# Kernel optimization log

Measured on AMD Instinct MI355X. Metric: run time of the kernel, lower is better.

Reference implementation:

```python
import jax, jax.numpy as jnp
import numpy as np

HEAD_DIM = 64
NUM_HEADS = 32
ROPE_BASE = 10000.0


def _rope_interleaved(x):
    # x: [B, T, H, D]; interleaved RoPE on query, seqlen_offset = 0
    B, T, H, D = x.shape
    inv_freq = 1.0 / (ROPE_BASE ** (jnp.arange(0, D, 2, dtype=jnp.float32) / D))  # [D/2]
    t = jnp.arange(T, dtype=jnp.float32)
    freqs = t[:, None] * inv_freq[None, :]          # [T, D/2]
    cos = jnp.cos(freqs)[None, :, None, :]          # [1, T, 1, D/2]
    sin = jnp.sin(freqs)[None, :, None, :]
    x1 = x[..., 0::2]
    x2 = x[..., 1::2]
    o1 = x1 * cos - x2 * sin
    o2 = x1 * sin + x2 * cos
    out = jnp.stack([o1, o2], axis=-1).reshape(x.shape)  # re-interleave
    return out


def setup_inputs() -> dict:
    key = jax.random.key(0)
    k1, k2, k3, k4, k5 = jax.random.split(key, 5)
    B, T, Dm = 2, 2048, 2048
    H, Dh = NUM_HEADS, HEAD_DIM
    scale = 0.02
    return {
        "hidden_states": jax.random.normal(k1, (B, T, Dm), jnp.float32),
        "shared_k": jax.random.normal(k2, (B, T, H, Dh), jnp.float32),
        "shared_v": jax.random.normal(k3, (B, T, H, Dh), jnp.float32),
        "Wq": jax.random.normal(k4, (Dm, Dm), jnp.float32) * scale,
        "Wo": jax.random.normal(k5, (Dm, Dm), jnp.float32) * scale,
    }


def reference(hidden_states, shared_k, shared_v, Wq, Wo):
    B, T, Dm = hidden_states.shape
    H, Dh = NUM_HEADS, HEAD_DIM
    # q projection (nn.Linear: x @ W.T)
    q = (hidden_states @ Wq.T).reshape(B, T, H, Dh)
    # rotary on q only (seqlen_offset = shared_k_len - q_len = 0)
    q = _rope_interleaved(q)
    # parallel causal attention over shared KV cache (window_size=None)
    scale = 1.0 / jnp.sqrt(jnp.asarray(Dh, jnp.float32))
    scores = jnp.einsum('bqhd,bkhd->bhqk', q, shared_k) * scale
    causal = jnp.tril(jnp.ones((T, T), dtype=bool))
    scores = jnp.where(causal[None, None], scores, -jnp.inf)
    p = jax.nn.softmax(scores, axis=-1)
    o = jnp.einsum('bhqk,bkhd->bqhd', p, shared_v)
    o = o.reshape(B, T, Dm)
    return o @ Wo.T
```

## Files before the change

### kernel.cpp

```cpp
#include <hip/hip_runtime.h>
#include <stdint.h>

typedef short short8 __attribute__((ext_vector_type(8)));
typedef float f32x4 __attribute__((ext_vector_type(4)));
typedef int int2v __attribute__((ext_vector_type(2)));
typedef int int4v __attribute__((ext_vector_type(4)));

#define QSCALE 0.1803368801111137f
#define FREQC 0.4152410118609203f

__device__ __forceinline__ float bf2f(unsigned short u) {
    union { unsigned int i; float f; } x; x.i = ((unsigned int)u) << 16; return x.f;
}
__device__ __forceinline__ unsigned short f2bf(float f) {
    union { float f; unsigned int i; } x; x.f = f;
    unsigned int i = x.i;
    unsigned int r = i + 0x7FFFu + ((i >> 16) & 1u);
    return (unsigned short)(r >> 16);
}
__device__ __forceinline__ ushort4 cvt4(float4 v) {
    ushort4 o;
    o.x = f2bf(v.x); o.y = f2bf(v.y); o.z = f2bf(v.z); o.w = f2bf(v.w);
    return o;
}
__device__ __forceinline__ int cvtpk_bf16(float lo, float hi) {
    int r;
    asm("v_cvt_pk_bf16_f32 %0, %1, %2" : "=v"(r) : "v"(lo), "v"(hi));
    return r;
}

#define GLDS16(g, l) \
    __builtin_amdgcn_global_load_lds((const __attribute__((address_space(1))) void*)(g), \
                                     (__attribute__((address_space(3))) void*)(l), 16, 0, 0)

#define WAITVM(n) asm volatile("s_waitcnt vmcnt(" #n ")" ::: "memory")

__global__ __launch_bounds__(256) void cvt_tr(
    const float* __restrict__ hs, const float* __restrict__ k,
    const float* __restrict__ wq, const float* __restrict__ wo,
    const float* __restrict__ V,
    unsigned short* __restrict__ hs_b, unsigned short* __restrict__ k_b,
    unsigned short* __restrict__ wq_b, unsigned short* __restrict__ wo_b,
    unsigned short* __restrict__ Vt) {
    __shared__ float s[64 * 65];
    int blk = blockIdx.x;
    int tid = threadIdx.x;
    if (blk < 2048) {
        size_t base = (size_t)blk * 256 + tid;
        const float4* inh = (const float4*)hs;
        const float4* ink = (const float4*)k;
        const float4* inq = (const float4*)wq;
        const float4* ino = (const float4*)wo;
        ushort4* outh = (ushort4*)hs_b;
        ushort4* outk = (ushort4*)k_b;
        ushort4* outq = (ushort4*)wq_b;
        ushort4* outo = (ushort4*)wo_b;
        {
            float4 v[4];
#pragma unroll
            for (int it = 0; it < 4; ++it) v[it] = inh[(size_t)it * 524288 + base];
#pragma unroll
            for (int it = 0; it < 4; ++it) outh[(size_t)it * 524288 + base] = cvt4(v[it]);
        }
        {
            float4 v[4];
#pragma unroll
            for (int it = 0; it < 4; ++it) v[it] = ink[(size_t)it * 524288 + base];
#pragma unroll
            for (int it = 0; it < 4; ++it) outk[(size_t)it * 524288 + base] = cvt4(v[it]);
        }
        {
            float4 v[2];
#pragma unroll
            for (int it = 0; it < 2; ++it) v[it] = inq[(size_t)it * 524288 + base];
#pragma unroll
            for (int it = 0; it < 2; ++it) outq[(size_t)it * 524288 + base] = cvt4(v[it]);
        }
        {
            float4 v[2];
#pragma unroll
            for (int it = 0; it < 2; ++it) v[it] = ino[(size_t)it * 524288 + base];
#pragma unroll
            for (int it = 0; it < 2; ++it) outo[(size_t)it * 524288 + base] = cvt4(v[it]);
        }
        return;
    }
    int tb = blk - 2048;
    int t0 = (tb & 31) * 64;
    int bh = tb >> 5;
    int b = bh >> 5, h = bh & 31;
#pragma unroll
    for (int it = 0; it < 4; ++it) {
        int c = tid + it * 256;
        int t = c >> 4;
        int d0 = (c & 15) * 4;
        float4 v = *(const float4*)(V + (size_t)(((b * 2048 + t0 + t) * 32 + h)) * 64 + d0);
        s[t * 65 + d0 + 0] = v.x; s[t * 65 + d0 + 1] = v.y;
        s[t * 65 + d0 + 2] = v.z; s[t * 65 + d0 + 3] = v.w;
    }
    __syncthreads();
#pragma unroll
    for (int it = 0; it < 2; ++it) {
        int c = tid + it * 256;
        int d = c >> 3;
        int tt = (c & 7) * 8;
        short8 pk;
#pragma unroll
        for (int j = 0; j < 8; ++j) pk[j] = (short)f2bf(s[(tt + j) * 65 + d]);
        *(short8*)(Vt + (size_t)(bh * 64 + d) * 2048 + t0 + tt) = pk;
    }
}

template <bool BF16_OUT>
__global__ __launch_bounds__(256) void gemm_bt(
    const unsigned short* __restrict__ A,
    const unsigned short* __restrict__ B,
    void* __restrict__ Cout,
    int M, int N, int K)
{
    __shared__ __align__(16) unsigned short lA[2][128 * 64];
    __shared__ __align__(16) unsigned short lB[2][128 * 64];
    int tid = threadIdx.x, lane = tid & 63, wave = tid >> 6;
    int wm = (wave >> 1) * 64, wn = (wave & 1) * 64;
    int m16 = lane & 15, q = lane >> 4;
    int rowBase = blockIdx.x * 128, colBase = blockIdx.y * 128;
    f32x4 acc[4][4] = {};

    int sr = lane >> 3;
    int g  = (lane & 7) ^ sr;
    const unsigned short* gAp = A + (size_t)(rowBase + wave * 32 + sr) * K + g * 8;
    const unsigned short* gBp = B + (size_t)(colBase + wave * 32 + sr) * K + g * 8;

#define GSTAGE(buf, k0)                                                                      \
    do {                                                                                     \
        _Pragma("unroll")                                                                    \
        for (int gi = 0; gi < 4; ++gi) {                                                     \
            GLDS16(gAp + (size_t)(8 * gi) * K + (k0), &lA[buf][(wave * 32 + 8 * gi) * 64]);  \
            GLDS16(gBp + (size_t)(8 * gi) * K + (k0), &lB[buf][(wave * 32 + 8 * gi) * 64]);  \
        }                                                                                    \
    } while (0)

    GSTAGE(0, 0);
    WAITVM(0);
    __builtin_amdgcn_s_barrier();
    int cur = 0;
    for (int k0 = 0; k0 < K; k0 += 64) {
        if (k0 + 64 < K) {
            GSTAGE(cur ^ 1, k0 + 64);
            WAITVM(8);
        } else {
            WAITVM(0);
        }
        __builtin_amdgcn_s_barrier();
        const unsigned short* la = lA[cur];
        const unsigned short* lb = lB[cur];
#pragma unroll
        for (int kk = 0; kk < 2; ++kk) {
            short8 af[4], bfr[4];
#pragma unroll
            for (int i2 = 0; i2 < 4; ++i2) {
                int RA = wm + i2 * 16 + m16;
                af[i2]  = *(const short8*)&la[RA * 64 + (((kk * 4 + q) ^ (RA & 7)) * 8)];
                int RB = wn + i2 * 16 + m16;
                bfr[i2] = *(const short8*)&lb[RB * 64 + (((kk * 4 + q) ^ (RB & 7)) * 8)];
            }
#pragma unroll
            for (int i2 = 0; i2 < 4; ++i2)
#pragma unroll
                for (int jn = 0; jn < 4; ++jn)
                    acc[i2][jn] = __builtin_amdgcn_mfma_f32_16x16x32_bf16(af[i2], bfr[jn], acc[i2][jn], 0, 0, 0);
        }
        __builtin_amdgcn_s_barrier();
        cur ^= 1;
    }
#pragma unroll
    for (int i = 0; i < 4; ++i)
#pragma unroll
        for (int jn = 0; jn < 4; ++jn)
#pragma unroll
            for (int r = 0; r < 4; ++r) {
                int row = rowBase + wm + i * 16 + q * 4 + r;
                int col = colBase + wn + jn * 16 + m16;
                float v = acc[i][jn][r];
                if (BF16_OUT) ((unsigned short*)Cout)[(size_t)row * N + col] = f2bf(v);
                else          ((float*)Cout)[(size_t)row * N + col] = v;
            }
}

__global__ __launch_bounds__(256, 4) void attn(
    const unsigned short* __restrict__ Q,
    const unsigned short* __restrict__ Kb,
    const unsigned short* __restrict__ Vt,
    unsigned short* __restrict__ O)
{
    __shared__ __align__(16) unsigned short sK[2][64 * 64];
    __shared__ __align__(16) unsigned short sV[2][64 * 64];
    int tid = threadIdx.x, lane = tid & 63, w = tid >> 6;
    int m16 = lane & 15, q = lane >> 4;
    int rx = m16 & 7;
    int flat = blockIdx.x;
    int bh = flat & 63, p = flat >> 6;
    int b = bh >> 5, h = bh & 31;
    int qtA = 31 - p, qtB = p;

    short8 aqA0, aqA1, aqB0, aqB1;
    {
        int tA = qtA * 64 + w * 16 + m16;
        int tB = qtB * 64 + w * 16 + m16;
        const unsigned short* rowA = Q + (size_t)(b * 2048 + tA) * 2048 + h * 64 + q * 8;
        const unsigned short* rowB = Q + (size_t)(b * 2048 + tB) * 2048 + h * 64 + q * 8;
        short8 a0 = *(const short8*)rowA, a1 = *(const short8*)(rowA + 32);
        short8 b0 = *(const short8*)rowB, b1 = *(const short8*)(rowB + 32);
        float tfA = (float)tA, tfB = (float)tB;
#pragma unroll
        for (int j = 0; j < 4; ++j) {
            float inv0 = __builtin_amdgcn_exp2f(-FREQC * (float)(q * 4 + j));
            float inv1 = __builtin_amdgcn_exp2f(-FREQC * (float)(16 + q * 4 + j));
            float cA0 = __cosf(tfA * inv0), sA0 = __sinf(tfA * inv0);
            float cA1 = __cosf(tfA * inv1), sA1 = __sinf(tfA * inv1);
            float cB0 = __cosf(tfB * inv0), sB0 = __sinf(tfB * inv0);
            float cB1 = __cosf(tfB * inv1), sB1 = __sinf(tfB * inv1);
            float x1, x2;
            x1 = bf2f((unsigned short)a0[2 * j]); x2 = bf2f((unsigned short)a0[2 * j + 1]);
            aqA0[2 * j]     = (short)f2bf((x1 * cA0 - x2 * sA0) * QSCALE);
            aqA0[2 * j + 1] = (short)f2bf((x1 * sA0 + x2 * cA0) * QSCALE);
            x1 = bf2f((unsigned short)a1[2 * j]); x2 = bf2f((unsigned short)a1[2 * j + 1]);
            aqA1[2 * j]     = (short)f2bf((x1 * cA1 - x2 * sA1) * QSCALE);
            aqA1[2 * j + 1] = (short)f2bf((x1 * sA1 + x2 * cA1) * QSCALE);
            x1 = bf2f((unsigned short)b0[2 * j]); x2 = bf2f((unsigned short)b0[2 * j + 1]);
            aqB0[2 * j]     = (short)f2bf((x1 * cB0 - x2 * sB0) * QSCALE);
            aqB0[2 * j + 1] = (short)f2bf((x1 * sB0 + x2 * cB0) * QSCALE);
            x1 = bf2f((unsigned short)b1[2 * j]); x2 = bf2f((unsigned short)b1[2 * j + 1]);
            aqB1[2 * j]     = (short)f2bf((x1 * cB1 - x2 * sB1) * QSCALE);
            aqB1[2 * j + 1] = (short)f2bf((x1 * sB1 + x2 * cB1) * QSCALE);
        }
    }

    float lrunA = 0.f, lrunB = 0.f;
    f32x4 accOA[4], accOB[4];
#pragma unroll
    for (int nt = 0; nt < 4; ++nt) {
        f32x4 z = {0.f, 0.f, 0.f, 0.f};
        accOA[nt] = z; accOB[nt] = z;
    }

    int sr = lane >> 3, g = (lane & 7) ^ sr;
    int rb = w * 16;
    const unsigned short* kgp = Kb + (size_t)(b * 2048 + rb + sr) * 2048 + h * 64 + g * 8;
    const unsigned short* vgp = Vt + (size_t)((b * 32 + h) * 64 + rb + sr) * 2048 + g * 8;

#define ASTAGE(kt, bi)                                                                \
    do {                                                                              \
        int kb0 = (kt) * 64;                                                          \
        _Pragma("unroll")                                                             \
        for (int gi = 0; gi < 2; ++gi) {                                              \
            GLDS16(kgp + (size_t)(kb0 + 8 * gi) * 2048, &sK[bi][(rb + 8 * gi) * 64]); \
            GLDS16(vgp + (size_t)(8 * gi) * 2048 + kb0, &sV[bi][(rb + 8 * gi) * 64]); \
        }                                                                             \
    } while (0)

    ASTAGE(0, 0);
    WAITVM(0);
    __builtin_amdgcn_s_barrier();
    int cur = 0;
    for (int kt = 0; kt <= qtA; ++kt) {
        if (kt < qtA) {
            ASTAGE(kt + 1, cur ^ 1);
            WAITVM(4);
        } else {
            WAITVM(0);
        }
        __builtin_amdgcn_s_barrier();
        bool doB = (kt <= qtB);
        bool diagA = (kt == qtA), diagB = (kt == qtB);
        const unsigned short* kbuf = sK[cur];
        const unsigned short* vbuf = sV[cur];

        int pkA[4][2], pkB[4][2];
#pragma unroll
        for (int nt = 0; nt < 4; ++nt) {
            const unsigned short* kr = kbuf + (nt * 16 + m16) * 64;
            short8 bk0 = *(const short8*)&kr[(q ^ rx) * 8];
            short8 bk1 = *(const short8*)&kr[((4 + q) ^ rx) * 8];
            f32x4 zA = {0.f, 0.f, 0.f, 0.f};
            zA = __builtin_amdgcn_mfma_f32_16x16x32_bf16(bk0, aqA0, zA, 0, 0, 0);
            zA = __builtin_amdgcn_mfma_f32_16x16x32_bf16(bk1, aqA1, zA, 0, 0, 0);
            float e[4];
#pragma unroll
            for (int r = 0; r < 4; ++r) {
                float s = zA[r];
                if (diagA && (nt * 16 + q * 4 + r > w * 16 + m16)) s = -__builtin_inff();
                e[r] = __builtin_amdgcn_exp2f(s);
            }
            lrunA += (e[0] + e[1]) + (e[2] + e[3]);
            pkA[nt][0] = cvtpk_bf16(e[0], e[1]);
            pkA[nt][1] = cvtpk_bf16(e[2], e[3]);
            if (doB) {
                f32x4 zB = {0.f, 0.f, 0.f, 0.f};
                zB = __builtin_amdgcn_mfma_f32_16x16x32_bf16(bk0, aqB0, zB, 0, 0, 0);
                zB = __builtin_amdgcn_mfma_f32_16x16x32_bf16(bk1, aqB1, zB, 0, 0, 0);
                float eb[4];
#pragma unroll
                for (int r = 0; r < 4; ++r) {
                    float s = zB[r];
                    if (diagB && (nt * 16 + q * 4 + r > w * 16 + m16)) s = -__builtin_inff();
                    eb[r] = __builtin_amdgcn_exp2f(s);
                }
                lrunB += (eb[0] + eb[1]) + (eb[2] + eb[3]);
                pkB[nt][0] = cvtpk_bf16(eb[0], eb[1]);
                pkB[nt][1] = cvtpk_bf16(eb[2], eb[3]);
            }
        }

        int4v tA0 = {pkA[0][0], pkA[0][1], pkA[1][0], pkA[1][1]};
        int4v tA1 = {pkA[2][0], pkA[2][1], pkA[3][0], pkA[3][1]};
        short8 apA0 = __builtin_bit_cast(short8, tA0);
        short8 apA1 = __builtin_bit_cast(short8, tA1);
        short8 apB0, apB1;
        if (doB) {
            int4v tB0 = {pkB[0][0], pkB[0][1], pkB[1][0], pkB[1][1]};
            int4v tB1 = {pkB[2][0], pkB[2][1], pkB[3][0], pkB[3][1]};
            apB0 = __builtin_bit_cast(short8, tB0);
            apB1 = __builtin_bit_cast(short8, tB1);
        }

#pragma unroll
        for (int nt = 0; nt < 4; ++nt) {
            const unsigned short* vr = vbuf + (nt * 16 + m16) * 64;
            int2v a0 = *(const int2v*)&vr[(((q >> 1) + 0) ^ rx) * 8 + (q & 1) * 4];
            int2v a1 = *(const int2v*)&vr[(((q >> 1) + 2) ^ rx) * 8 + (q & 1) * 4];
            int2v a2 = *(const int2v*)&vr[(((q >> 1) + 4) ^ rx) * 8 + (q & 1) * 4];
            int2v a3 = *(const int2v*)&vr[(((q >> 1) + 6) ^ rx) * 8 + (q & 1) * 4];
            int4v tv0 = {a0.x, a0.y, a1.x, a1.y};
            int4v tv1 = {a2.x, a2.y, a3.x, a3.y};
            short8 bv0 = __builtin_bit_cast(short8, tv0);
            short8 bv1 = __builtin_bit_cast(short8, tv1);
            accOA[nt] = __builtin_amdgcn_mfma_f32_16x16x32_bf16(apA0, bv0, accOA[nt], 0, 0, 0);
            accOA[nt] = __builtin_amdgcn_mfma_f32_16x16x32_bf16(apA1, bv1, accOA[nt], 0, 0, 0);
            if (doB) {
                accOB[nt] = __builtin_amdgcn_mfma_f32_16x16x32_bf16(apB0, bv0, accOB[nt], 0, 0, 0);
                accOB[nt] = __builtin_amdgcn_mfma_f32_16x16x32_bf16(apB1, bv1, accOB[nt], 0, 0, 0);
            }
        }
        __builtin_amdgcn_s_barrier();
        cur ^= 1;
    }

    lrunA += __shfl_xor(lrunA, 16); lrunA += __shfl_xor(lrunA, 32);
    lrunB += __shfl_xor(lrunB, 16); lrunB += __shfl_xor(lrunB, 32);
    float invA = 1.0f / lrunA, invB = 1.0f / lrunB;
    float nA[4], nB[4];
#pragma unroll
    for (int r = 0; r < 4; ++r) {
        nA[r] = __shfl(invA, q * 4 + r);
        nB[r] = __shfl(invB, q * 4 + r);
    }
#pragma unroll
    for (int nt = 0; nt < 4; ++nt)
#pragma unroll
        for (int r = 0; r < 4; ++r) {
            int col = h * 64 + nt * 16 + m16;
            O[(size_t)(b * 2048 + qtA * 64 + w * 16 + q * 4 + r) * 2048 + col] =
                f2bf(accOA[nt][r] * nA[r]);
            O[(size_t)(b * 2048 + qtB * 64 + w * 16 + q * 4 + r) * 2048 + col] =
                f2bf(accOB[nt][r] * nB[r]);
        }
}

extern "C" void kernel_launch(void* const* d_in, const int* in_sizes, int n_in,
                              void* d_out, int out_size, void* d_ws, size_t ws_size,
                              hipStream_t stream) {
    const float* hs = (const float*)d_in[0];
    const float* sk = (const float*)d_in[1];
    const float* sv = (const float*)d_in[2];
    const float* wq = (const float*)d_in[3];
    const float* wo = (const float*)d_in[4];
    float* out = (float*)d_out;

    char* ws = (char*)d_ws;
    unsigned short* hid_b = (unsigned short*)(ws);
    unsigned short* wq_b  = (unsigned short*)(ws + ((size_t)16 << 20));
    unsigned short* wo_b  = (unsigned short*)(ws + ((size_t)24 << 20));
    unsigned short* k_b   = (unsigned short*)(ws + ((size_t)32 << 20));
    unsigned short* vt_b  = (unsigned short*)(ws + ((size_t)48 << 20));
    unsigned short* q_b   = (unsigned short*)(ws + ((size_t)64 << 20));
    unsigned short* o_b   = (unsigned short*)(ws + ((size_t)80 << 20));

    cvt_tr<<<4096, 256, 0, stream>>>(hs, sk, wq, wo, sv, hid_b, k_b, wq_b, wo_b, vt_b);
    gemm_bt<true><<<dim3(32, 16), 256, 0, stream>>>(hid_b, wq_b, (void*)q_b, 4096, 2048, 2048);
    attn<<<1024, 256, 0, stream>>>(q_b, k_b, vt_b, o_b);
    gemm_bt<false><<<dim3(32, 16), 256, 0, stream>>>(o_b, wo_b, (void*)out, 4096, 2048, 2048);
}
```

Measured before the change: 294.5 us.

## Triple-buffer attention K/V tiles and split conversion kernel into two launches

The attention kernel moves from two to three LDS buffers for K and V, which removes the trailing barrier at the end of each iteration and lowers the occupancy hint from 4 to 3 blocks. The fused convert/transpose kernel is split into a simple one-float4-per-thread conversion kernel with 24576 blocks and a separate V transpose kernel. The aim is to cut barrier stalls in attention, at the cost of more LDS per block and one extra kernel launch. Dropping the barrier relies on a three-deep ring being enough to avoid overwriting a buffer that slower waves are still reading.

```diff
diff --git a/kernel.cpp b/kernel.cpp
--- a/kernel.cpp
+++ b/kernel.cpp
@@ -18,11 +18,6 @@
     unsigned int r = i + 0x7FFFu + ((i >> 16) & 1u);
     return (unsigned short)(r >> 16);
 }
-__device__ __forceinline__ ushort4 cvt4(float4 v) {
-    ushort4 o;
-    o.x = f2bf(v.x); o.y = f2bf(v.y); o.z = f2bf(v.z); o.w = f2bf(v.w);
-    return o;
-}
 __device__ __forceinline__ int cvtpk_bf16(float lo, float hi) {
     int r;
     asm("v_cvt_pk_bf16_f32 %0, %1, %2" : "=v"(r) : "v"(lo), "v"(hi));
@@ -35,60 +30,28 @@
 
 #define WAITVM(n) asm volatile("s_waitcnt vmcnt(" #n ")" ::: "memory")
 
-__global__ __launch_bounds__(256) void cvt_tr(
-    const float* __restrict__ hs, const float* __restrict__ k,
-    const float* __restrict__ wq, const float* __restrict__ wo,
-    const float* __restrict__ V,
-    unsigned short* __restrict__ hs_b, unsigned short* __restrict__ k_b,
-    unsigned short* __restrict__ wq_b, unsigned short* __restrict__ wo_b,
-    unsigned short* __restrict__ Vt) {
+__global__ void cvt_all(const float* __restrict__ hs, const float* __restrict__ k,
+                        const float* __restrict__ wq, const float* __restrict__ wo,
+                        unsigned short* __restrict__ hs_b, unsigned short* __restrict__ k_b,
+                        unsigned short* __restrict__ wq_b, unsigned short* __restrict__ wo_b) {
+    int blk = blockIdx.x;
+    const float* in; unsigned short* out; int i;
+    if (blk < 8192)        { in = hs; out = hs_b; i = blk * 256 + threadIdx.x; }
+    else if (blk < 16384)  { in = k;  out = k_b;  i = (blk - 8192) * 256 + threadIdx.x; }
+    else if (blk < 20480)  { in = wq; out = wq_b; i = (blk - 16384) * 256 + threadIdx.x; }
+    else                   { in = wo; out = wo_b; i = (blk - 20480) * 256 + threadIdx.x; }
+    float4 v = ((const float4*)in)[i];
+    ushort4 o;
+    o.x = f2bf(v.x); o.y = f2bf(v.y); o.z = f2bf(v.z); o.w = f2bf(v.w);
+    ((ushort4*)out)[i] = o;
+}
+
+__global__ __launch_bounds__(256) void transpose_v(const float* __restrict__ V, unsigned short* __restrict__ Vt) {
     __shared__ float s[64 * 65];
-    int blk = blockIdx.x;
+    int t0 = blockIdx.x * 64;
+    int bh = blockIdx.y;
+    int b = bh >> 5, h = bh & 31;
     int tid = threadIdx.x;
-    if (blk < 2048) {
-        size_t base = (size_t)blk * 256 + tid;
-        const float4* inh = (const float4*)hs;
-        const float4* ink = (const float4*)k;
-        const float4* inq = (const float4*)wq;
-        const float4* ino = (const float4*)wo;
-        ushort4* outh = (ushort4*)hs_b;
-        ushort4* outk = (ushort4*)k_b;
-        ushort4* outq = (ushort4*)wq_b;
-        ushort4* outo = (ushort4*)wo_b;
-        {
-            float4 v[4];
-#pragma unroll
-            for (int it = 0; it < 4; ++it) v[it] = inh[(size_t)it * 524288 + base];
-#pragma unroll
-            for (int it = 0; it < 4; ++it) outh[(size_t)it * 524288 + base] = cvt4(v[it]);
-        }
-        {
-            float4 v[4];
-#pragma unroll
-            for (int it = 0; it < 4; ++it) v[it] = ink[(size_t)it * 524288 + base];
-#pragma unroll
-            for (int it = 0; it < 4; ++it) outk[(size_t)it * 524288 + base] = cvt4(v[it]);
-        }
-        {
-            float4 v[2];
-#pragma unroll
-            for (int it = 0; it < 2; ++it) v[it] = inq[(size_t)it * 524288 + base];
-#pragma unroll
-            for (int it = 0; it < 2; ++it) outq[(size_t)it * 524288 + base] = cvt4(v[it]);
-        }
-        {
-            float4 v[2];
-#pragma unroll
-            for (int it = 0; it < 2; ++it) v[it] = ino[(size_t)it * 524288 + base];
-#pragma unroll
-            for (int it = 0; it < 2; ++it) outo[(size_t)it * 524288 + base] = cvt4(v[it]);
-        }
-        return;
-    }
-    int tb = blk - 2048;
-    int t0 = (tb & 31) * 64;
-    int bh = tb >> 5;
-    int b = bh >> 5, h = bh & 31;
 #pragma unroll
     for (int it = 0; it < 4; ++it) {
         int c = tid + it * 256;
@@ -187,14 +150,14 @@
             }
 }
 
-__global__ __launch_bounds__(256, 4) void attn(
+__global__ __launch_bounds__(256, 3) void attn(
     const unsigned short* __restrict__ Q,
     const unsigned short* __restrict__ Kb,
     const unsigned short* __restrict__ Vt,
     unsigned short* __restrict__ O)
 {
-    __shared__ __align__(16) unsigned short sK[2][64 * 64];
-    __shared__ __align__(16) unsigned short sV[2][64 * 64];
+    __shared__ __align__(16) unsigned short sK[3][64 * 64];
+    __shared__ __align__(16) unsigned short sV[3][64 * 64];
     int tid = threadIdx.x, lane = tid & 63, w = tid >> 6;
     int m16 = lane & 15, q = lane >> 4;
     int rx = m16 & 7;
@@ -262,10 +225,10 @@
     ASTAGE(0, 0);
     WAITVM(0);
     __builtin_amdgcn_s_barrier();
-    int cur = 0;
+    int cur = 0, nxt = 1;
     for (int kt = 0; kt <= qtA; ++kt) {
         if (kt < qtA) {
-            ASTAGE(kt + 1, cur ^ 1);
+            ASTAGE(kt + 1, nxt);
             WAITVM(4);
         } else {
             WAITVM(0);
@@ -342,8 +305,8 @@
                 accOB[nt] = __builtin_amdgcn_mfma_f32_16x16x32_bf16(apB1, bv1, accOB[nt], 0, 0, 0);
             }
         }
-        __builtin_amdgcn_s_barrier();
-        cur ^= 1;
+        cur = (cur == 2) ? 0 : cur + 1;
+        nxt = (nxt == 2) ? 0 : nxt + 1;
     }
 
     lrunA += __shfl_xor(lrunA, 16); lrunA += __shfl_xor(lrunA, 32);
@@ -386,7 +349,8 @@
     unsigned short* q_b   = (unsigned short*)(ws + ((size_t)64 << 20));
     unsigned short* o_b   = (unsigned short*)(ws + ((size_t)80 << 20));
 
-    cvt_tr<<<4096, 256, 0, stream>>>(hs, sk, wq, wo, sv, hid_b, k_b, wq_b, wo_b, vt_b);
+    cvt_all<<<24576, 256, 0, stream>>>(hs, sk, wq, wo, hid_b, k_b, wq_b, wo_b);
+    transpose_v<<<dim3(32, 64), 256, 0, stream>>>(sv, vt_b);
     gemm_bt<true><<<dim3(32, 16), 256, 0, stream>>>(hid_b, wq_b, (void*)q_b, 4096, 2048, 2048);
     attn<<<1024, 256, 0, stream>>>(q_b, k_b, vt_b, o_b);
     gemm_bt<false><<<dim3(32, 16), 256, 0, stream>>>(o_b, wo_b, (void*)out, 4096, 2048, 2048);
```

Result: no change. 297.5 us (+1.0%).
